# Kernel optimization log

Measured on AMD Instinct MI355X. Metric: run time of the kernel, lower is better.

## Reference

```python
import jax, jax.numpy as jnp
import numpy as np

NUM_EXPERTS = 64
TOP_K = 2
DIM = 4096
TOKENS = 16384


def setup_inputs() -> dict:
    key = jax.random.key(0)
    k1, k2 = jax.random.split(key)
    x = jax.random.normal(k1, (TOKENS, DIM), dtype=jnp.float32)
    # nn.Linear weight: [num_experts, dim], scaled like kaiming-uniform-ish init
    w_gating = jax.random.normal(k2, (NUM_EXPERTS, DIM), dtype=jnp.float32) * (1.0 / np.sqrt(DIM))
    return {"x": x, "w_gating": w_gating}


def reference(x, w_gating):
    # gating linear (no bias, noise=0 / eval mode)
    logits = jnp.einsum("td,ed->te", x, w_gating)          # [tokens, experts]
    scores = jax.nn.softmax(logits, axis=-1)                # [tokens, experts]
    topk_scores, topk_experts = jax.lax.top_k(scores, TOP_K)  # [tokens, top_k]
    combine_weight = topk_scores
    me = scores.mean(axis=0)                                # [experts]
    ce = (scores > 0).astype(jnp.float32).mean(axis=0)      # [experts]
    load_balance_loss = (me * ce).sum() * NUM_EXPERTS
    z_loss = (jax.nn.logsumexp(logits, axis=-1) ** 2).mean()
    return topk_experts, combine_weight, scores, load_balance_loss, z_loss
```

## Files before the change

### kernel.cpp

```cpp
#include <hip/hip_runtime.h>
#include <hip/hip_bf16.h>

typedef __attribute__((ext_vector_type(8))) short bf16x8;
typedef __attribute__((ext_vector_type(4))) float f32x4;

#define N_TOKENS 16384
#define DIM 4096
#define TOKB 32
#define BK 128
#define NIT (DIM / BK)
#define NBUF 4
#define BUF_F (TOKB * BK)
#define N_EXP 64

#define OFF_W   (N_TOKENS * 2)
#define OFF_S   (N_TOKENS * 4)
#define OFF_LBL (N_TOKENS * 4 + N_TOKENS * N_EXP)
#define OFF_Z   (OFF_LBL + 1)

#define WS_WHI_F 512
#define WS_WLO_F (512 + (N_EXP * DIM) / 2)

typedef const __attribute__((address_space(1))) void GV;
typedef __attribute__((address_space(3))) void LV;

__device__ __forceinline__ unsigned int pkhi(float a, float b) {
  return __builtin_amdgcn_perm(__float_as_uint(b), __float_as_uint(a), 0x07060302u);
}
__device__ __forceinline__ float resid(float f) {
  return f - __uint_as_float(__float_as_uint(f) & 0xFFFF0000u);
}
__device__ __forceinline__ void tsplit8(const f32x4 p0, const f32x4 p1,
                                        bf16x8& hi, bf16x8& lo) {
  uint4 H = make_uint4(pkhi(p0[0], p0[1]), pkhi(p0[2], p0[3]),
                       pkhi(p1[0], p1[1]), pkhi(p1[2], p1[3]));
  float r0 = resid(p0[0]), r1 = resid(p0[1]), r2 = resid(p0[2]), r3 = resid(p0[3]);
  float r4 = resid(p1[0]), r5 = resid(p1[1]), r6 = resid(p1[2]), r7 = resid(p1[3]);
  uint4 L = make_uint4(pkhi(r0, r1), pkhi(r2, r3), pkhi(r4, r5), pkhi(r6, r7));
  hi = __builtin_bit_cast(bf16x8, H);
  lo = __builtin_bit_cast(bf16x8, L);
}

__global__ __launch_bounds__(256) void split_w_kernel(
    const float* __restrict__ w,
    unsigned short* __restrict__ whi, unsigned short* __restrict__ wlo)
{
  const int i = blockIdx.x * 256 + threadIdx.x;
  const int e = i >> 12, k = i & 4095;
  float f = w[i];
  unsigned short h = __builtin_bit_cast(unsigned short, __float2bfloat16(f));
  float hf = __uint_as_float(((unsigned)h) << 16);
  unsigned short l = __builtin_bit_cast(unsigned short, __float2bfloat16(f - hf));
  const int q = e >> 5, n = (e >> 4) & 1, r15 = e & 15;
  const int it = k >> 7, kq = (k >> 5) & 3, half = (k >> 3) & 3, j = k & 7;
  const int lane = half * 16 + r15;
  const int idx = (((kq * 2 + q) * 32 + it) * 1024) + n * 512 + lane * 8 + j;
  whi[idx] = h;
  wlo[idx] = l;
}

__global__ __launch_bounds__(512, 4) void router_kernel(
    const float* __restrict__ x,
    const unsigned short* __restrict__ whi, const unsigned short* __restrict__ wlo,
    float* __restrict__ out, float* __restrict__ ws)
{
  __shared__ __align__(16) float smem[NBUF * BUF_F];

  const int tid  = threadIdx.x;
  const int lane = tid & 63;
  const int wv   = __builtin_amdgcn_readfirstlane(tid >> 6);
  const int q    = wv & 1;
  const int kq   = wv >> 1;
  const int half = lane >> 4;
  const int r15  = lane & 15;
  const int tok0 = blockIdx.x * TOKB;

  const int row0 = wv * 4 + (lane >> 5);
  const int row1 = row0 + 2;
  const int sU   = lane & 31;
  const float* g0 = x + (size_t)(tok0 + row0) * DIM + ((sU ^ (row0 & 7)) << 2);
  const float* g1 = x + (size_t)(tok0 + row1) * DIM + ((sU ^ (row1 & 7)) << 2);
  float* const ldst = smem + wv * 512;

#define STAGE(buf, it_) do {                                                  \
    const float* s0_ = g0 + (size_t)(it_) * BK;                               \
    const float* s1_ = g1 + (size_t)(it_) * BK;                               \
    float* d_ = ldst + (buf) * BUF_F;                                         \
    __builtin_amdgcn_global_load_lds((GV*)s0_, (LV*)d_,       16, 0, 0);      \
    __builtin_amdgcn_global_load_lds((GV*)s1_, (LV*)(d_+256), 16, 0, 0);      \
  } while (0)

  const unsigned short* wph = whi + ((kq * 2 + q) << 15);
  const unsigned short* wpl = wlo + ((kq * 2 + q) << 15);
  const int lo16 = lane * 8;

  f32x4 acc[2][2];
#pragma unroll
  for (int tt = 0; tt < 2; ++tt)
#pragma unroll
    for (int n = 0; n < 2; ++n) acc[tt][n] = (f32x4){0.f, 0.f, 0.f, 0.f};

#define COMPUTE(itc, BH0, BH1, BL0, BL1) do {                                  \
    const float* bufp = smem + ((itc) & 3) * BUF_F;                            \
    _Pragma("unroll")                                                          \
    for (int tt = 0; tt < 2; ++tt) {                                           \
      const int rowA = tt * 16 + r15;                                          \
      const int g    = r15 & 7;                                                \
      const float* rp = bufp + rowA * BK;                                      \
      const int u0 = kq * 8 + ((half * 2) ^ g);                                \
      const int u1 = kq * 8 + ((half * 2 + 1) ^ g);                            \
      f32x4 p0 = *(const f32x4*)(rp + (u0 << 2));                              \
      f32x4 p1 = *(const f32x4*)(rp + (u1 << 2));                              \
      bf16x8 ah, al;                                                           \
      tsplit8(p0, p1, ah, al);                                                 \
      acc[tt][0] = __builtin_amdgcn_mfma_f32_16x16x32_bf16(ah, BH0, acc[tt][0], 0, 0, 0); \
      acc[tt][0] = __builtin_amdgcn_mfma_f32_16x16x32_bf16(al, BH0, acc[tt][0], 0, 0, 0); \
      acc[tt][0] = __builtin_amdgcn_mfma_f32_16x16x32_bf16(ah, BL0, acc[tt][0], 0, 0, 0); \
      acc[tt][1] = __builtin_amdgcn_mfma_f32_16x16x32_bf16(ah, BH1, acc[tt][1], 0, 0, 0); \
      acc[tt][1] = __builtin_amdgcn_mfma_f32_16x16x32_bf16(al, BH1, acc[tt][1], 0, 0, 0); \
      acc[tt][1] = __builtin_amdgcn_mfma_f32_16x16x32_bf16(ah, BL1, acc[tt][1], 0, 0, 0); \
    }                                                                          \
  } while (0)

  STAGE(0, 0);
  STAGE(1, 1);

  for (int s = 0; s < NIT / 2; ++s) {
    const int it0 = 2 * s, it1 = 2 * s + 1;

    const unsigned short* ph0 = wph + it0 * 1024;
    const unsigned short* pl0 = wpl + it0 * 1024;
    const unsigned short* ph1 = wph + it1 * 1024;
    const unsigned short* pl1 = wpl + it1 * 1024;
    bf16x8 Abh0 = *(const bf16x8*)(ph0 + lo16);
    bf16x8 Abh1 = *(const bf16x8*)(ph0 + 512 + lo16);
    bf16x8 Abl0 = *(const bf16x8*)(pl0 + lo16);
    bf16x8 Abl1 = *(const bf16x8*)(pl0 + 512 + lo16);
    bf16x8 Bbh0 = *(const bf16x8*)(ph1 + lo16);
    bf16x8 Bbh1 = *(const bf16x8*)(ph1 + 512 + lo16);
    bf16x8 Bbl0 = *(const bf16x8*)(pl1 + lo16);
    bf16x8 Bbl1 = *(const bf16x8*)(pl1 + 512 + lo16);

    asm volatile("s_waitcnt vmcnt(8)" ::: "memory");
    __builtin_amdgcn_s_barrier();

    STAGE((it0 + 2) & 3, (it0 + 2 < NIT) ? it0 + 2 : NIT - 1);
    STAGE((it1 + 2) & 3, (it1 + 2 < NIT) ? it1 + 2 : NIT - 1);

    COMPUTE(it0, Abh0, Abh1, Abl0, Abl1);
    COMPUTE(it1, Bbh0, Bbh1, Bbl0, Bbl1);
  }

  asm volatile("s_waitcnt vmcnt(0)" ::: "memory");
  __syncthreads();

  float* lb = smem;
  {
    float* dst = lb + kq * (TOKB * 65);
#pragma unroll
    for (int tt = 0; tt < 2; ++tt) {
#pragma unroll
      for (int n = 0; n < 2; ++n) {
#pragma unroll
        for (int r = 0; r < 4; ++r) {
          dst[(tt * 16 + half * 4 + r) * 65 + q * 32 + n * 16 + r15] = acc[tt][n][r];
        }
      }
    }
  }
  __syncthreads();

  for (int i = tid; i < TOKB * 64; i += 512) {
    const int t = i >> 6, e = i & 63;
    lb[t * 65 + e] += lb[2080 + t * 65 + e] + lb[4160 + t * 65 + e] + lb[6240 + t * 65 + e];
  }
  __syncthreads();

  if (wv == 0 && lane < TOKB) {
    const int token = tok0 + lane;
    float v[64];
#pragma unroll
    for (int e = 0; e < 64; ++e) v[e] = lb[lane * 65 + e];
    float m = v[0];
#pragma unroll
    for (int e = 1; e < 64; ++e) m = fmaxf(m, v[e]);
    float sum = 0.f;
#pragma unroll
    for (int e = 0; e < 64; ++e) { v[e] = expf(v[e] - m); sum += v[e]; }
    const float inv = 1.0f / sum;
    float m1 = -1.f, m2 = -1.f;
    int   i1 = 0,    i2 = 0;
#pragma unroll
    for (int e = 0; e < 64; ++e) {
      float sc = v[e] * inv;
      lb[lane * 65 + e] = sc;
      if (sc > m1)      { m2 = m1; i2 = i1; m1 = sc; i1 = e; }
      else if (sc > m2) { m2 = sc; i2 = e; }
    }
    out[2 * token]         = (float)i1;
    out[2 * token + 1]     = (float)i2;
    out[OFF_W + 2 * token]     = m1;
    out[OFF_W + 2 * token + 1] = m2;

    float lse = m + logf(sum);
    float z = lse * lse;
#pragma unroll
    for (int off = 16; off > 0; off >>= 1) z += __shfl_down(z, off);
    if (lane == 0) atomicAdd(ws + 128, z);
  }
  __syncthreads();

  float* outS = out + OFF_S + (size_t)blockIdx.x * TOKB * 64;
  for (int i = tid; i < TOKB * 64; i += 512) {
    outS[i] = lb[(i >> 6) * 65 + (i & 63)];
  }

  if (wv == 0) {
    float sm = 0.f, cn = 0.f;
#pragma unroll
    for (int t = 0; t < TOKB; ++t) {
      float sc = lb[t * 65 + lane];
      sm += sc;
      cn += (sc > 0.f) ? 1.f : 0.f;
    }
    atomicAdd(ws + lane, sm);
    atomicAdd(ws + 64 + lane, cn);
  }
#undef STAGE
#undef COMPUTE
}

__global__ void finalize_kernel(const float* __restrict__ ws, float* __restrict__ out) {
  const int l = threadIdx.x;
  const float invT = 1.0f / (float)N_TOKENS;
  float me = ws[l] * invT;
  float ce = ws[64 + l] * invT;
  float p = me * ce;
#pragma unroll
  for (int off = 32; off > 0; off >>= 1) p += __shfl_down(p, off);
  if (l == 0) {
    out[OFF_LBL] = p * (float)N_EXP;
    out[OFF_Z]   = ws[128] * invT;
  }
}

extern "C" void kernel_launch(void* const* d_in, const int* in_sizes, int n_in,
                              void* d_out, int out_size, void* d_ws, size_t ws_size,
                              hipStream_t stream) {
  const float* x = (const float*)d_in[0];
  const float* w = (const float*)d_in[1];
  float* out = (float*)d_out;
  float* ws  = (float*)d_ws;
  unsigned short* whi = (unsigned short*)(ws + WS_WHI_F);
  unsigned short* wlo = (unsigned short*)(ws + WS_WLO_F);

  (void)hipMemsetAsync(d_ws, 0, 129 * sizeof(float), stream);
  split_w_kernel<<<(N_EXP * DIM) / 256, 256, 0, stream>>>(w, whi, wlo);
  router_kernel<<<N_TOKENS / TOKB, 512, 0, stream>>>(x, whi, wlo, out, ws);
  finalize_kernel<<<1, 64, 0, stream>>>(ws, out);
}
```

Before: 84.40 us.

## Restage tiles as 16 tokens by 256 K so weight fragments serve both token halves

```diff
diff --git a/kernel.cpp b/kernel.cpp
--- a/kernel.cpp
+++ b/kernel.cpp
@@ -7,10 +7,9 @@
 #define N_TOKENS 16384
 #define DIM 4096
 #define TOKB 32
-#define BK 128
-#define NIT (DIM / BK)
+#define NIT 32
 #define NBUF 4
-#define BUF_F (TOKB * BK)
+#define BUF_F (16 * 256)
 #define N_EXP 64
 
 #define OFF_W   (N_TOKENS * 2)
@@ -52,9 +51,10 @@
   float hf = __uint_as_float(((unsigned)h) << 16);
   unsigned short l = __builtin_bit_cast(unsigned short, __float2bfloat16(f - hf));
   const int q = e >> 5, n = (e >> 4) & 1, r15 = e & 15;
-  const int it = k >> 7, kq = (k >> 5) & 3, half = (k >> 3) & 3, j = k & 7;
+  const int kc = k >> 8, kq = (k >> 6) & 3, j = (k >> 5) & 1, half = (k >> 3) & 3,
+            jj = k & 7;
   const int lane = half * 16 + r15;
-  const int idx = (((kq * 2 + q) * 32 + it) * 1024) + n * 512 + lane * 8 + j;
+  const int idx = ((kq * 2 + q) << 15) + kc * 2048 + (j * 2 + n) * 512 + lane * 8 + jj;
   whi[idx] = h;
   wlo[idx] = l;
 }
@@ -73,18 +73,21 @@
   const int kq   = wv >> 1;
   const int half = lane >> 4;
   const int r15  = lane & 15;
+  const int g8   = r15 & 7;
   const int tok0 = blockIdx.x * TOKB;
 
-  const int row0 = wv * 4 + (lane >> 5);
-  const int row1 = row0 + 2;
-  const int sU   = lane & 31;
-  const float* g0 = x + (size_t)(tok0 + row0) * DIM + ((sU ^ (row0 & 7)) << 2);
-  const float* g1 = x + (size_t)(tok0 + row1) * DIM + ((sU ^ (row1 & 7)) << 2);
+  const int rl0 = 2 * wv, rl1 = 2 * wv + 1;
+  const float* gs00 = x + (size_t)(tok0 + rl0) * DIM      + ((lane ^ (rl0 & 7)) << 2);
+  const float* gs01 = x + (size_t)(tok0 + rl1) * DIM      + ((lane ^ (rl1 & 7)) << 2);
+  const float* gs10 = x + (size_t)(tok0 + 16 + rl0) * DIM + ((lane ^ (rl0 & 7)) << 2);
+  const float* gs11 = x + (size_t)(tok0 + 16 + rl1) * DIM + ((lane ^ (rl1 & 7)) << 2);
   float* const ldst = smem + wv * 512;
 
 #define STAGE(buf, it_) do {                                                  \
-    const float* s0_ = g0 + (size_t)(it_) * BK;                               \
-    const float* s1_ = g1 + (size_t)(it_) * BK;                               \
+    const int rh_ = (it_) & 1;                                                \
+    const size_t ko_ = (size_t)((it_) >> 1) * 256;                            \
+    const float* s0_ = (rh_ ? gs10 : gs00) + ko_;                             \
+    const float* s1_ = (rh_ ? gs11 : gs01) + ko_;                             \
     float* d_ = ldst + (buf) * BUF_F;                                         \
     __builtin_amdgcn_global_load_lds((GV*)s0_, (LV*)d_,       16, 0, 0);      \
     __builtin_amdgcn_global_load_lds((GV*)s1_, (LV*)(d_+256), 16, 0, 0);      \
@@ -94,31 +97,42 @@
   const unsigned short* wpl = wlo + ((kq * 2 + q) << 15);
   const int lo16 = lane * 8;
 
-  f32x4 acc[2][2];
-#pragma unroll
-  for (int tt = 0; tt < 2; ++tt)
-#pragma unroll
-    for (int n = 0; n < 2; ++n) acc[tt][n] = (f32x4){0.f, 0.f, 0.f, 0.f};
-
-#define COMPUTE(itc, BH0, BH1, BL0, BL1) do {                                  \
-    const float* bufp = smem + ((itc) & 3) * BUF_F;                            \
-    _Pragma("unroll")                                                          \
-    for (int tt = 0; tt < 2; ++tt) {                                           \
-      const int rowA = tt * 16 + r15;                                          \
-      const int g    = r15 & 7;                                                \
-      const float* rp = bufp + rowA * BK;                                      \
-      const int u0 = kq * 8 + ((half * 2) ^ g);                                \
-      const int u1 = kq * 8 + ((half * 2 + 1) ^ g);                            \
+  f32x4 acc0[2], acc1[2];
+#pragma unroll
+  for (int n = 0; n < 2; ++n) {
+    acc0[n] = (f32x4){0.f, 0.f, 0.f, 0.f};
+    acc1[n] = (f32x4){0.f, 0.f, 0.f, 0.f};
+  }
+
+#define COMPUTE(itc, ACC, H00, H01, H10, H11, L00, L01, L10, L11) do {         \
+    const float* rp = smem + ((itc) & 3) * BUF_F + r15 * 256;                  \
+     {                                                              \
+      const int u0 = kq * 16 + ((half * 2) ^ g8);                              \
+      const int u1 = kq * 16 + ((half * 2 + 1) ^ g8);                          \
       f32x4 p0 = *(const f32x4*)(rp + (u0 << 2));                              \
       f32x4 p1 = *(const f32x4*)(rp + (u1 << 2));                              \
       bf16x8 ah, al;                                                           \
       tsplit8(p0, p1, ah, al);                                                 \
-      acc[tt][0] = __builtin_amdgcn_mfma_f32_16x16x32_bf16(ah, BH0, acc[tt][0], 0, 0, 0); \
-      acc[tt][0] = __builtin_amdgcn_mfma_f32_16x16x32_bf16(al, BH0, acc[tt][0], 0, 0, 0); \
-      acc[tt][0] = __builtin_amdgcn_mfma_f32_16x16x32_bf16(ah, BL0, acc[tt][0], 0, 0, 0); \
-      acc[tt][1] = __builtin_amdgcn_mfma_f32_16x16x32_bf16(ah, BH1, acc[tt][1], 0, 0, 0); \
-      acc[tt][1] = __builtin_amdgcn_mfma_f32_16x16x32_bf16(al, BH1, acc[tt][1], 0, 0, 0); \
-      acc[tt][1] = __builtin_amdgcn_mfma_f32_16x16x32_bf16(ah, BL1, acc[tt][1], 0, 0, 0); \
+      ACC[0] = __builtin_amdgcn_mfma_f32_16x16x32_bf16(ah, H00, ACC[0], 0, 0, 0); \
+      ACC[0] = __builtin_amdgcn_mfma_f32_16x16x32_bf16(al, H00, ACC[0], 0, 0, 0); \
+      ACC[0] = __builtin_amdgcn_mfma_f32_16x16x32_bf16(ah, L00, ACC[0], 0, 0, 0); \
+      ACC[1] = __builtin_amdgcn_mfma_f32_16x16x32_bf16(ah, H01, ACC[1], 0, 0, 0); \
+      ACC[1] = __builtin_amdgcn_mfma_f32_16x16x32_bf16(al, H01, ACC[1], 0, 0, 0); \
+      ACC[1] = __builtin_amdgcn_mfma_f32_16x16x32_bf16(ah, L01, ACC[1], 0, 0, 0); \
+    }                                                                          \
+     {                                                              \
+      const int u0 = kq * 16 + 8 + ((half * 2) ^ g8);                          \
+      const int u1 = kq * 16 + 8 + ((half * 2 + 1) ^ g8);                      \
+      f32x4 p0 = *(const f32x4*)(rp + (u0 << 2));                              \
+      f32x4 p1 = *(const f32x4*)(rp + (u1 << 2));                              \
+      bf16x8 ah, al;                                                           \
+      tsplit8(p0, p1, ah, al);                                                 \
+      ACC[0] = __builtin_amdgcn_mfma_f32_16x16x32_bf16(ah, H10, ACC[0], 0, 0, 0); \
+      ACC[0] = __builtin_amdgcn_mfma_f32_16x16x32_bf16(al, H10, ACC[0], 0, 0, 0); \
+      ACC[0] = __builtin_amdgcn_mfma_f32_16x16x32_bf16(ah, L10, ACC[0], 0, 0, 0); \
+      ACC[1] = __builtin_amdgcn_mfma_f32_16x16x32_bf16(ah, H11, ACC[1], 0, 0, 0); \
+      ACC[1] = __builtin_amdgcn_mfma_f32_16x16x32_bf16(al, H11, ACC[1], 0, 0, 0); \
+      ACC[1] = __builtin_amdgcn_mfma_f32_16x16x32_bf16(ah, L11, ACC[1], 0, 0, 0); \
     }                                                                          \
   } while (0)
 
@@ -128,27 +142,27 @@
   for (int s = 0; s < NIT / 2; ++s) {
     const int it0 = 2 * s, it1 = 2 * s + 1;
 
-    const unsigned short* ph0 = wph + it0 * 1024;
-    const unsigned short* pl0 = wpl + it0 * 1024;
-    const unsigned short* ph1 = wph + it1 * 1024;
-    const unsigned short* pl1 = wpl + it1 * 1024;
-    bf16x8 Abh0 = *(const bf16x8*)(ph0 + lo16);
-    bf16x8 Abh1 = *(const bf16x8*)(ph0 + 512 + lo16);
-    bf16x8 Abl0 = *(const bf16x8*)(pl0 + lo16);
-    bf16x8 Abl1 = *(const bf16x8*)(pl0 + 512 + lo16);
-    bf16x8 Bbh0 = *(const bf16x8*)(ph1 + lo16);
-    bf16x8 Bbh1 = *(const bf16x8*)(ph1 + 512 + lo16);
-    bf16x8 Bbl0 = *(const bf16x8*)(pl1 + lo16);
-    bf16x8 Bbl1 = *(const bf16x8*)(pl1 + 512 + lo16);
-
-    asm volatile("s_waitcnt vmcnt(8)" ::: "memory");
+    const unsigned short* ph = wph + s * 2048;
+    const unsigned short* pl = wpl + s * 2048;
+    bf16x8 H00 = *(const bf16x8*)(ph + lo16);
+    bf16x8 H01 = *(const bf16x8*)(ph + 512 + lo16);
+    bf16x8 H10 = *(const bf16x8*)(ph + 1024 + lo16);
+    bf16x8 H11 = *(const bf16x8*)(ph + 1536 + lo16);
+    bf16x8 L00 = *(const bf16x8*)(pl + lo16);
+    bf16x8 L01 = *(const bf16x8*)(pl + 512 + lo16);
+    bf16x8 L10 = *(const bf16x8*)(pl + 1024 + lo16);
+    bf16x8 L11 = *(const bf16x8*)(pl + 1536 + lo16);
+
+    STAGE((it0 + 2) & 3, (it0 + 2 < NIT) ? it0 + 2 : NIT - 1);
+
+    asm volatile("s_waitcnt vmcnt(12)" ::: "memory");
     __builtin_amdgcn_s_barrier();
-
-    STAGE((it0 + 2) & 3, (it0 + 2 < NIT) ? it0 + 2 : NIT - 1);
+    COMPUTE(it0, acc0, H00, H01, H10, H11, L00, L01, L10, L11);
+
     STAGE((it1 + 2) & 3, (it1 + 2 < NIT) ? it1 + 2 : NIT - 1);
-
-    COMPUTE(it0, Abh0, Abh1, Abl0, Abl1);
-    COMPUTE(it1, Bbh0, Bbh1, Bbl0, Bbl1);
+    asm volatile("s_waitcnt vmcnt(4)" ::: "memory");
+    __builtin_amdgcn_s_barrier();
+    COMPUTE(it1, acc1, H00, H01, H10, H11, L00, L01, L10, L11);
   }
 
   asm volatile("s_waitcnt vmcnt(0)" ::: "memory");
@@ -158,13 +172,11 @@
   {
     float* dst = lb + kq * (TOKB * 65);
 #pragma unroll
-    for (int tt = 0; tt < 2; ++tt) {
-#pragma unroll
-      for (int n = 0; n < 2; ++n) {
-#pragma unroll
-        for (int r = 0; r < 4; ++r) {
-          dst[(tt * 16 + half * 4 + r) * 65 + q * 32 + n * 16 + r15] = acc[tt][n][r];
-        }
+    for (int n = 0; n < 2; ++n) {
+#pragma unroll
+      for (int r = 0; r < 4; ++r) {
+        dst[(half * 4 + r) * 65 + q * 32 + n * 16 + r15]      = acc0[n][r];
+        dst[(16 + half * 4 + r) * 65 + q * 32 + n * 16 + r15] = acc1[n][r];
       }
     }
   }
```

Result: faster. 81.78 us (median of 2 runs) (-3.1%).
